# Performance work log

Hardware: AMD Instinct MI355X
Metric: run time of the kernel (lower is better)

## Reference

```python
import jax, jax.numpy as jnp
import numpy as np

BINS = 8

def setup_inputs() -> dict:
    key = jax.random.key(0)
    k1, k2, k3 = jax.random.split(key, 3)
    B, H, W = 32, 160, 160
    HW = H * W
    reg_logits = jax.random.normal(k1, (B, 4 * BINS, H, W), dtype=jnp.float32)
    targets = jax.random.uniform(k2, (B, HW, 4), dtype=jnp.float32) * (BINS - 1)
    pos_mask = jax.random.randint(k3, (B, HW), 0, 2) == 1
    return {"reg_logits": reg_logits, "targets": targets, "pos_mask": pos_mask}

def reference(reg_logits, targets, pos_mask):
    bins = BINS
    B, C, H, W = reg_logits.shape
    HW = H * W
    # [B, C, H, W] -> [B, HW, 4, bins]
    rl = reg_logits.transpose(0, 2, 3, 1).reshape(B, HW, 4, bins)
    t = jnp.clip(targets, 0.0, bins - 1 - 0.0001)          # [B, HW, 4]
    l_id = jnp.floor(t).astype(jnp.int32)
    u_id = jnp.minimum(l_id + 1, bins - 1)
    w_u = t - l_id.astype(t.dtype)
    w_l = 1.0 - w_u
    logp = jax.nn.log_softmax(rl, axis=-1)                 # [B, HW, 4, bins]
    nll_l = -jnp.take_along_axis(logp, l_id[..., None], axis=-1)[..., 0]
    nll_u = -jnp.take_along_axis(logp, u_id[..., None], axis=-1)[..., 0]
    per = w_l * nll_l + w_u * nll_u                        # [B, HW, 4]
    m = pos_mask.astype(per.dtype)                         # [B, HW]
    npos = jnp.sum(m)
    # mean over positives per coordinate, averaged over 4 coords ==
    # sum over (positives x 4) / (npos * 4)
    total = jnp.sum(per * m[..., None])
    loss = total / (jnp.maximum(npos, 1.0) * 4.0)
    return jnp.where(npos > 0, loss, jnp.zeros((), dtype=per.dtype))
```

## Files before the change

kernel.cpp:

```cpp
#include <hip/hip_runtime.h>

#define BINS 8
#define BLOCK 256

__global__ void init_acc_kernel(float* acc) {
    acc[0] = 0.0f;
    acc[1] = 0.0f;
}

__device__ __forceinline__ float comp4(const float4& v, int i) {
    return (i == 0) ? v.x : (i == 1) ? v.y : (i == 2) ? v.z : v.w;
}

__global__ __launch_bounds__(BLOCK) void dfl_main_kernel(
    const float* __restrict__ logits,
    const float* __restrict__ targets,
    const int*   __restrict__ mask,
    float* __restrict__ acc,
    int B, int HW) {

    const int g = blockIdx.x * BLOCK + threadIdx.x;
    const int ngroups = B * (HW >> 2);

    float tsum = 0.0f;
    float tcnt = 0.0f;

    if (g < ngroups) {
        const int p4 = g << 2;
        const int b  = p4 / HW;
        const int pp = p4 - b * HW;

        const float* base = logits + (size_t)b * 4 * BINS * HW + pp;

        const float4* tgt = (const float4*)(targets + (size_t)p4 * 4);
        float4 t4[4];
#pragma unroll
        for (int i = 0; i < 4; ++i) t4[i] = tgt[i];

        const int4 mk = *(const int4*)(mask + p4);
        float msk[4];
        msk[0] = mk.x ? 1.0f : 0.0f;
        msk[1] = mk.y ? 1.0f : 0.0f;
        msk[2] = mk.z ? 1.0f : 0.0f;
        msk[3] = mk.w ? 1.0f : 0.0f;
        tcnt = msk[0] + msk[1] + msk[2] + msk[3];

#pragma unroll
        for (int c = 0; c < 4; ++c) {
            float4 xv[BINS];
#pragma unroll
            for (int j = 0; j < BINS; ++j)
                xv[j] = *(const float4*)(base + (size_t)(c * BINS + j) * HW);

#pragma unroll
            for (int i = 0; i < 4; ++i) {
                float x[BINS];
#pragma unroll
                for (int j = 0; j < BINS; ++j) x[j] = comp4(xv[j], i);

                float t = comp4(t4[i], c);
                t = fminf(fmaxf(t, 0.0f), (float)(BINS - 1) - 0.0001f);
                float lf = floorf(t);
                int   li = (int)lf;
                int   ui = li + 1;
                float wu = t - lf;
                float wl = 1.0f - wu;

                float m = x[0];
#pragma unroll
                for (int j = 1; j < BINS; ++j) m = fmaxf(m, x[j]);
                float s = 0.0f;
#pragma unroll
                for (int j = 0; j < BINS; ++j) s += __expf(x[j] - m);
                float lse = m + __logf(s);

                float xl = x[0], xu = x[0];
#pragma unroll
                for (int j = 1; j < BINS; ++j) {
                    xl = (li == j) ? x[j] : xl;
                    xu = (ui == j) ? x[j] : xu;
                }

                float per = lse - (wl * xl + wu * xu);
                tsum += msk[i] * per;
            }
        }
    }

#pragma unroll
    for (int off = 32; off > 0; off >>= 1) {
        tsum += __shfl_down(tsum, off, 64);
        tcnt += __shfl_down(tcnt, off, 64);
    }

    __shared__ float ssum[BLOCK / 64];
    __shared__ float scnt[BLOCK / 64];
    const int wid  = threadIdx.x >> 6;
    const int lane = threadIdx.x & 63;
    if (lane == 0) { ssum[wid] = tsum; scnt[wid] = tcnt; }
    __syncthreads();
    if (threadIdx.x == 0) {
        float bs = 0.0f, bc = 0.0f;
#pragma unroll
        for (int w = 0; w < BLOCK / 64; ++w) { bs += ssum[w]; bc += scnt[w]; }
        atomicAdd(&acc[0], bs);
        atomicAdd(&acc[1], bc);
    }
}

__global__ void finalize_kernel(const float* __restrict__ acc,
                                float* __restrict__ out) {
    float total = acc[0];
    float npos  = acc[1];
    float loss  = total / (fmaxf(npos, 1.0f) * 4.0f);
    out[0] = (npos > 0.0f) ? loss : 0.0f;
}

extern "C" void kernel_launch(void* const* d_in, const int* in_sizes, int n_in,
                              void* d_out, int out_size, void* d_ws, size_t ws_size,
                              hipStream_t stream) {
    const float* logits  = (const float*)d_in[0];
    const float* targets = (const float*)d_in[1];
    const int*   mask    = (const int*)d_in[2];
    float* out = (float*)d_out;
    float* acc = (float*)d_ws;

    const int B  = 32;
    const int HW = 160 * 160;

    init_acc_kernel<<<1, 1, 0, stream>>>(acc);

    const int ngroups = B * (HW / 4);
    const int nblocks = (ngroups + BLOCK - 1) / BLOCK;
    dfl_main_kernel<<<nblocks, BLOCK, 0, stream>>>(logits, targets, mask, acc, B, HW);

    finalize_kernel<<<1, 1, 0, stream>>>(acc, out);
}
```

Measured before the change: 178.5 us.

## Use persistent grid-stride kernel, fuse finalize via last-block counter, drop max in softmax

```diff
diff --git a/kernel.cpp b/kernel.cpp
--- a/kernel.cpp
+++ b/kernel.cpp
@@ -2,10 +2,16 @@
 
 #define BINS 8
 #define BLOCK 256
+#define NB 768
+
+constexpr int BATCH   = 32;
+constexpr int HW      = 25600;
+constexpr int NGROUPS = BATCH * HW / 4;
 
 __global__ void init_acc_kernel(float* acc) {
     acc[0] = 0.0f;
     acc[1] = 0.0f;
+    ((unsigned*)acc)[2] = 0u;
 }
 
 __device__ __forceinline__ float comp4(const float4& v, int i) {
@@ -17,15 +23,12 @@
     const float* __restrict__ targets,
     const int*   __restrict__ mask,
     float* __restrict__ acc,
-    int B, int HW) {
-
-    const int g = blockIdx.x * BLOCK + threadIdx.x;
-    const int ngroups = B * (HW >> 2);
+    float* __restrict__ out) {
 
     float tsum = 0.0f;
     float tcnt = 0.0f;
 
-    if (g < ngroups) {
+    for (int g = blockIdx.x * BLOCK + threadIdx.x; g < NGROUPS; g += NB * BLOCK) {
         const int p4 = g << 2;
         const int b  = p4 / HW;
         const int pp = p4 - b * HW;
@@ -43,7 +46,7 @@
         msk[1] = mk.y ? 1.0f : 0.0f;
         msk[2] = mk.z ? 1.0f : 0.0f;
         msk[3] = mk.w ? 1.0f : 0.0f;
-        tcnt = msk[0] + msk[1] + msk[2] + msk[3];
+        tcnt += msk[0] + msk[1] + msk[2] + msk[3];
 
 #pragma unroll
         for (int c = 0; c < 4; ++c) {
@@ -66,13 +69,10 @@
                 float wu = t - lf;
                 float wl = 1.0f - wu;
 
-                float m = x[0];
-#pragma unroll
-                for (int j = 1; j < BINS; ++j) m = fmaxf(m, x[j]);
                 float s = 0.0f;
 #pragma unroll
-                for (int j = 0; j < BINS; ++j) s += __expf(x[j] - m);
-                float lse = m + __logf(s);
+                for (int j = 0; j < BINS; ++j) s += __expf(x[j]);
+                float lse = __logf(s);
 
                 float xl = x[0], xu = x[0];
 #pragma unroll
@@ -81,8 +81,7 @@
                     xu = (ui == j) ? x[j] : xu;
                 }
 
-                float per = lse - (wl * xl + wu * xu);
-                tsum += msk[i] * per;
+                tsum += msk[i] * (lse - (wl * xl + wu * xu));
             }
         }
     }
@@ -99,21 +98,22 @@
     const int lane = threadIdx.x & 63;
     if (lane == 0) { ssum[wid] = tsum; scnt[wid] = tcnt; }
     __syncthreads();
+
     if (threadIdx.x == 0) {
         float bs = 0.0f, bc = 0.0f;
 #pragma unroll
         for (int w = 0; w < BLOCK / 64; ++w) { bs += ssum[w]; bc += scnt[w]; }
         atomicAdd(&acc[0], bs);
         atomicAdd(&acc[1], bc);
+        __threadfence();
+        unsigned done = atomicAdd((unsigned*)acc + 2, 1u);
+        if (done == NB - 1) {
+            float total = atomicAdd(&acc[0], 0.0f);
+            float npos  = atomicAdd(&acc[1], 0.0f);
+            float loss  = total / (fmaxf(npos, 1.0f) * 4.0f);
+            out[0] = (npos > 0.0f) ? loss : 0.0f;
+        }
     }
-}
-
-__global__ void finalize_kernel(const float* __restrict__ acc,
-                                float* __restrict__ out) {
-    float total = acc[0];
-    float npos  = acc[1];
-    float loss  = total / (fmaxf(npos, 1.0f) * 4.0f);
-    out[0] = (npos > 0.0f) ? loss : 0.0f;
 }
 
 extern "C" void kernel_launch(void* const* d_in, const int* in_sizes, int n_in,
@@ -125,14 +125,6 @@
     float* out = (float*)d_out;
     float* acc = (float*)d_ws;
 
-    const int B  = 32;
-    const int HW = 160 * 160;
-
     init_acc_kernel<<<1, 1, 0, stream>>>(acc);
-
-    const int ngroups = B * (HW / 4);
-    const int nblocks = (ngroups + BLOCK - 1) / BLOCK;
-    dfl_main_kernel<<<nblocks, BLOCK, 0, stream>>>(logits, targets, mask, acc, B, HW);
-
-    finalize_kernel<<<1, 1, 0, stream>>>(acc, out);
+    dfl_main_kernel<<<NB, BLOCK, 0, stream>>>(logits, targets, mask, acc, out);
 }
```

Result: slower. 203.8 us (+14.1%).
